# Optimization experiments

Measured on AMD Instinct MI355X. Metric: run time of the kernel, lower is better.

## Reference

```python
import jax, jax.numpy as jnp
import numpy as np

GRID = 20            # grid_size -> n1 = 400 nodes
CTX = 64             # context_size
HID = 10 * CTX       # hidden_dim per module code
BATCH = 256
K_ITERS = 100        # Dykstra iterations approximating the exact QP solve
LEAKY_SLOPE = 0.1


def _grid_incidence(g):
    """Incidence matrix of g x g grid DAG with right/down edges (SPO benchmark)."""
    n1 = g * g
    edges = []
    for i in range(g):
        for j in range(g):
            u = i * g + j
            if j + 1 < g:
                edges.append((u, u + 1))   # right
            if i + 1 < g:
                edges.append((u, u + g))   # down
    n2 = len(edges)
    A = np.zeros((n1, n2), dtype=np.float32)
    for e, (u, v) in enumerate(edges):
        A[u, e] = 1.0    # flow leaves u
        A[v, e] = -1.0   # flow enters v
    b = np.zeros(n1, dtype=np.float32)
    b[0] = 1.0           # source
    b[-1] = -1.0         # sink
    return A, b


def setup_inputs() -> dict:
    key = jax.random.key(0)
    ks = jax.random.split(key, 5)
    A_np, b_np = _grid_incidence(GRID)
    n2 = A_np.shape[1]
    d = jax.random.normal(ks[0], (BATCH, CTX), dtype=jnp.float32)
    W1 = jax.random.normal(ks[1], (CTX, HID), dtype=jnp.float32) / np.sqrt(CTX)
    b1 = jax.random.normal(ks[2], (HID,), dtype=jnp.float32) * 0.01
    W2 = jax.random.normal(ks[3], (HID, n2), dtype=jnp.float32) / np.sqrt(HID)
    b2 = jax.random.normal(ks[4], (n2,), dtype=jnp.float32) * 0.01
    return {
        "d": d, "W1": W1, "b1": b1, "W2": W2, "b2": b2,
        "A": jnp.asarray(A_np), "b_eq": jnp.asarray(b_np),
    }


def _solve_qp(w, A, b_eq):
    """Batched min_x w'x + 0.5||x||^2 s.t. Ax=b, x>=0 == proj of -w onto the
    feasible set, via Dykstra alternating projections (affine set / orthant)."""
    M = jnp.linalg.pinv(A @ A.T)  # [n1, n1]; AA' is the grid Laplacian (rank n1-1)

    def proj_affine(x):           # x: [B, n2]
        resid = x @ A.T - b_eq    # [B, n1]
        return x - (resid @ M) @ A

    y0 = -w                       # point to project
    p0 = jnp.zeros_like(w)
    q0 = jnp.zeros_like(w)

    def step(carry, _):
        y, p, q = carry
        t = y + p
        yp = proj_affine(t)
        p = t - yp
        t2 = yp + q
        y = jnp.maximum(t2, 0.0)  # projection onto x >= 0
        q = t2 - y
        return (y, p, q), None

    (y, _, _), _ = jax.lax.scan(step, (y0, p0, q0), None, length=K_ITERS)
    return y


def reference(d, W1, b1, W2, b2, A, b_eq):
    h = d @ W1 + b1
    h = jnp.where(h > 0, h, LEAKY_SLOPE * h)   # LeakyReLU(0.1)
    w = h @ W2 + b2                            # predicted edge costs [B, n2]
    return _solve_qp(w, A, b_eq)               # training-mode output: QP solution
```

## Files before the change

kernel.cpp:

```cpp
#include <hip/hip_runtime.h>
#include <math.h>

#define G 20
#define N1 400
#define N2 760
#define CTXS 64
#define HID 640
#define NB 256
#define ITERS 100
#define PI_D 3.14159265358979323846

__global__ __launch_bounds__(256, 1) void spnet_kernel(
    const float* __restrict__ dmat, const float* __restrict__ W1,
    const float* __restrict__ b1v, const float* __restrict__ W2,
    const float* __restrict__ b2v, const float* __restrict__ beq,
    float* __restrict__ out)
{
  const int tid = threadIdx.x;
  const int bb  = blockIdx.x;

  __shared__ __align__(16) float sV[N1];
  __shared__ __align__(16) float sdrow[CTXS];
  __shared__ __align__(16) float sh[HID];
  __shared__ __align__(16) float st0[N2];
  __shared__ __align__(16) float tRs[G][G];
  __shared__ __align__(16) float tDs[21][G];
  __shared__ __align__(16) float srow[G][G];
  __shared__ __align__(16) float T1T[G][G];
  __shared__ __align__(16) float T2T[G][G];
  __shared__ __align__(16) float W3m[G][G];
  __shared__ __align__(16) float Zs[G][G];

  for (int t = tid; t < N1; t += 256) {
    int k = t / G, i = t - G * k;
    double nk = (k == 0) ? 0.22360679774997896 : 0.31622776601683794;
    sV[t] = (float)(nk * cos(PI_D * (double)(k * (2 * i + 1)) / 40.0));
    ((float*)tRs)[t] = 0.f;
  }
  for (int t = tid; t < 21 * G; t += 256) ((float*)tDs)[t] = 0.f;
  if (tid < CTXS) sdrow[tid] = dmat[bb * CTXS + tid];
  __syncthreads();

  if (tid < HID / 4) {
    float4 acc = *(const float4*)(b1v + 4 * tid);
#pragma unroll 4
    for (int k = 0; k < CTXS; k += 4) {
      float4 h4 = *(const float4*)(sdrow + k);
      const float* wb = W1 + k * HID + 4 * tid;
      float4 w0 = *(const float4*)(wb);
      float4 w1 = *(const float4*)(wb + HID);
      float4 w2 = *(const float4*)(wb + 2 * HID);
      float4 w3 = *(const float4*)(wb + 3 * HID);
      acc.x = fmaf(h4.x, w0.x, acc.x); acc.y = fmaf(h4.x, w0.y, acc.y);
      acc.z = fmaf(h4.x, w0.z, acc.z); acc.w = fmaf(h4.x, w0.w, acc.w);
      acc.x = fmaf(h4.y, w1.x, acc.x); acc.y = fmaf(h4.y, w1.y, acc.y);
      acc.z = fmaf(h4.y, w1.z, acc.z); acc.w = fmaf(h4.y, w1.w, acc.w);
      acc.x = fmaf(h4.z, w2.x, acc.x); acc.y = fmaf(h4.z, w2.y, acc.y);
      acc.z = fmaf(h4.z, w2.z, acc.z); acc.w = fmaf(h4.z, w2.w, acc.w);
      acc.x = fmaf(h4.w, w3.x, acc.x); acc.y = fmaf(h4.w, w3.y, acc.y);
      acc.z = fmaf(h4.w, w3.z, acc.z); acc.w = fmaf(h4.w, w3.w, acc.w);
    }
    acc.x = acc.x > 0.f ? acc.x : 0.1f * acc.x;
    acc.y = acc.y > 0.f ? acc.y : 0.1f * acc.y;
    acc.z = acc.z > 0.f ? acc.z : 0.1f * acc.z;
    acc.w = acc.w > 0.f ? acc.w : 0.1f * acc.w;
    *(float4*)(sh + 4 * tid) = acc;
  }
  __syncthreads();

  if (tid < N2 / 4) {
    float4 acc = *(const float4*)(b2v + 4 * tid);
#pragma unroll 2
    for (int k = 0; k < HID; k += 4) {
      float4 h4 = *(const float4*)(sh + k);
      const float* wb = W2 + k * N2 + 4 * tid;
      float4 w0 = *(const float4*)(wb);
      float4 w1 = *(const float4*)(wb + N2);
      float4 w2 = *(const float4*)(wb + 2 * N2);
      float4 w3 = *(const float4*)(wb + 3 * N2);
      acc.x = fmaf(h4.x, w0.x, acc.x); acc.y = fmaf(h4.x, w0.y, acc.y);
      acc.z = fmaf(h4.x, w0.z, acc.z); acc.w = fmaf(h4.x, w0.w, acc.w);
      acc.x = fmaf(h4.y, w1.x, acc.x); acc.y = fmaf(h4.y, w1.y, acc.y);
      acc.z = fmaf(h4.y, w1.z, acc.z); acc.w = fmaf(h4.y, w1.w, acc.w);
      acc.x = fmaf(h4.z, w2.x, acc.x); acc.y = fmaf(h4.z, w2.y, acc.y);
      acc.z = fmaf(h4.z, w2.z, acc.z); acc.w = fmaf(h4.z, w2.w, acc.w);
      acc.x = fmaf(h4.w, w3.x, acc.x); acc.y = fmaf(h4.w, w3.y, acc.y);
      acc.z = fmaf(h4.w, w3.z, acc.z); acc.w = fmaf(h4.w, w3.w, acc.w);
    }
    float4 s; s.x = -acc.x; s.y = -acc.y; s.z = -acc.z; s.w = -acc.w;
    *(float4*)(st0 + 4 * tid) = s;
  }
  __syncthreads();

  const bool isD = (tid < 100);
  const int  rid = tid - 128;
  const bool isR = (rid >= 0 && rid < 100);

  const int dx  = tid % G;
  const int dk0 = 4 * (tid / G);
  float Vr[4][G], Vc[4][G], Sv[4];
  if (isD) {
#pragma unroll
    for (int a = 0; a < 4; ++a) {
      int k = dk0 + a;
#pragma unroll
      for (int m = 0; m < G; ++m) { Vr[a][m] = sV[k * G + m]; Vc[a][m] = sV[m * G + k]; }
      double lk = 2.0 - 2.0 * cos(PI_D * (double)k / 20.0);
      double lx = 2.0 - 2.0 * cos(PI_D * (double)dx / 20.0);
      Sv[a] = (k == 0 && dx == 0) ? 0.f : (float)(1.0 / (lk + lx));
    }
  }

  const int di = tid / 5, dj4 = (tid % 5) * 4;
  const bool dAct = isD && (di < 19);
  float dT[4], dQ[4], dY[4];
  if (dAct) {
#pragma unroll
    for (int m = 0; m < 4; ++m) {
      int j = dj4 + m;
      int e = (j < 19) ? (39 * di + 2 * j + 1) : (39 * di + 38);
      dT[m] = st0[e]; dQ[m] = 0.f; dY[m] = 0.f;
    }
    float4 w4 = {dT[0], dT[1], dT[2], dT[3]};
    *(float4*)&tDs[di + 1][dj4] = w4;
  }

  const int ri = rid / 5, rj4 = (rid % 5) * 4;
  float rT[4], rQ[4], rY[4]; float4 bq4 = {0.f, 0.f, 0.f, 0.f};
  if (isR) {
#pragma unroll
    for (int m = 0; m < 4; ++m) {
      int j = rj4 + m;
      if (j < 19) {
        int e = (ri < 19) ? (39 * ri + 2 * j) : (741 + j);
        rT[m] = st0[e];
      } else rT[m] = 0.f;
      rQ[m] = 0.f; rY[m] = 0.f;
    }
    float4 w4 = {rT[0], rT[1], rT[2], rT[3]};
    *(float4*)&tRs[ri][rj4] = w4;
    bq4 = *(const float4*)(beq + ri * G + rj4);
  }
  __syncthreads();

  for (int it = 0; it < ITERS; ++it) {
    if (isR) {
      float4 oR = *(const float4*)&tRs[ri][rj4];
      float  lf = (rj4 > 0) ? tRs[ri][rj4 - 1] : 0.f;
      float4 oD = *(const float4*)&tDs[ri + 1][rj4];
      float4 iD = *(const float4*)&tDs[ri][rj4];
      float4 r4;
      r4.x = oR.x + oD.x - lf   - iD.x - bq4.x;
      r4.y = oR.y + oD.y - oR.x - iD.y - bq4.y;
      r4.z = oR.z + oD.z - oR.y - iD.z - bq4.z;
      r4.w = oR.w + oD.w - oR.z - iD.w - bq4.w;
      *(float4*)&srow[ri][rj4] = r4;
    }
    __syncthreads();

    if (isD) {
      const float4* Rp = (const float4*)&srow[dx][0];
      float4 a0 = Rp[0], a1 = Rp[1], a2 = Rp[2], a3 = Rp[3], a4 = Rp[4];
      float rr[G] = {a0.x,a0.y,a0.z,a0.w, a1.x,a1.y,a1.z,a1.w, a2.x,a2.y,a2.z,a2.w,
                     a3.x,a3.y,a3.z,a3.w, a4.x,a4.y,a4.z,a4.w};
#pragma unroll
      for (int a = 0; a < 4; ++a) {
        float acc = 0.f;
#pragma unroll
        for (int m = 0; m < G; ++m) acc = fmaf(Vr[a][m], rr[m], acc);
        T1T[dk0 + a][dx] = acc;
      }
    }
    __syncthreads();

    if (isD) {
      const float4* Rp = (const float4*)&T1T[dx][0];
      float4 a0 = Rp[0], a1 = Rp[1], a2 = Rp[2], a3 = Rp[3], a4 = Rp[4];
      float rr[G] = {a0.x,a0.y,a0.z,a0.w, a1.x,a1.y,a1.z,a1.w, a2.x,a2.y,a2.z,a2.w,
                     a3.x,a3.y,a3.z,a3.w, a4.x,a4.y,a4.z,a4.w};
      float o[4];
#pragma unroll
      for (int a = 0; a < 4; ++a) {
        float acc = 0.f;
#pragma unroll
        for (int m = 0; m < G; ++m) acc = fmaf(Vr[a][m], rr[m], acc);
        o[a] = acc * Sv[a];
      }
      float4 w4 = {o[0], o[1], o[2], o[3]};
      *(float4*)&T2T[dx][dk0] = w4;
    }
    __syncthreads();

    if (isD) {
      const float4* Rp = (const float4*)&T2T[dx][0];
      float4 a0 = Rp[0], a1 = Rp[1], a2 = Rp[2], a3 = Rp[3], a4 = Rp[4];
      float rr[G] = {a0.x,a0.y,a0.z,a0.w, a1.x,a1.y,a1.z,a1.w, a2.x,a2.y,a2.z,a2.w,
                     a3.x,a3.y,a3.z,a3.w, a4.x,a4.y,a4.z,a4.w};
#pragma unroll
      for (int a = 0; a < 4; ++a) {
        float acc = 0.f;
#pragma unroll
        for (int m = 0; m < G; ++m) acc = fmaf(Vc[a][m], rr[m], acc);
        W3m[dk0 + a][dx] = acc;
      }
    }
    __syncthreads();

    if (isD) {
      const float4* Rp = (const float4*)&W3m[dx][0];
      float4 a0 = Rp[0], a1 = Rp[1], a2 = Rp[2], a3 = Rp[3], a4 = Rp[4];
      float rr[G] = {a0.x,a0.y,a0.z,a0.w, a1.x,a1.y,a1.z,a1.w, a2.x,a2.y,a2.z,a2.w,
                     a3.x,a3.y,a3.z,a3.w, a4.x,a4.y,a4.z,a4.w};
      float o[4];
#pragma unroll
      for (int a = 0; a < 4; ++a) {
        float acc = 0.f;
#pragma unroll
        for (int m = 0; m < G; ++m) acc = fmaf(Vc[a][m], rr[m], acc);
        o[a] = acc;
      }
      float4 w4 = {o[0], o[1], o[2], o[3]};
      *(float4*)&Zs[dx][dk0] = w4;
    }
    __syncthreads();

    if (isR) {
      float4 z4 = *(const float4*)&Zs[ri][rj4];
      float  zR = (rj4 < 16) ? Zs[ri][rj4 + 4] : 0.f;
      float pn[4] = {z4.x - z4.y, z4.y - z4.z, z4.z - z4.w, z4.w - zR};
      if (rj4 == 16) pn[3] = 0.f;
#pragma unroll
      for (int m = 0; m < 4; ++m) {
        float t2 = rT[m] - pn[m] + rQ[m];
        float yn = fmaxf(t2, 0.f);
        rQ[m] = t2 - yn; rY[m] = yn; rT[m] = yn + pn[m];
      }
      float4 w4 = {rT[0], rT[1], rT[2], rT[3]};
      *(float4*)&tRs[ri][rj4] = w4;
    }
    if (dAct) {
      float4 z4 = *(const float4*)&Zs[di][dj4];
      float4 zb = *(const float4*)&Zs[di + 1][dj4];
      float pn[4] = {z4.x - zb.x, z4.y - zb.y, z4.z - zb.z, z4.w - zb.w};
#pragma unroll
      for (int m = 0; m < 4; ++m) {
        float t2 = dT[m] - pn[m] + dQ[m];
        float yn = fmaxf(t2, 0.f);
        dQ[m] = t2 - yn; dY[m] = yn; dT[m] = yn + pn[m];
      }
      float4 w4 = {dT[0], dT[1], dT[2], dT[3]};
      *(float4*)&tDs[di + 1][dj4] = w4;
    }
    __syncthreads();
  }

  if (isR) {
#pragma unroll
    for (int m = 0; m < 4; ++m) {
      int j = rj4 + m;
      if (j < 19) {
        int e = (ri < 19) ? (39 * ri + 2 * j) : (741 + j);
        out[bb * N2 + e] = rY[m];
      }
    }
  }
  if (dAct) {
#pragma unroll
    for (int m = 0; m < 4; ++m) {
      int j = dj4 + m;
      int e = (j < 19) ? (39 * di + 2 * j + 1) : (39 * di + 38);
      out[bb * N2 + e] = dY[m];
    }
  }
}

extern "C" void kernel_launch(void* const* d_in, const int* in_sizes, int n_in,
                              void* d_out, int out_size, void* d_ws, size_t ws_size,
                              hipStream_t stream) {
  const float* d   = (const float*)d_in[0];
  const float* W1  = (const float*)d_in[1];
  const float* b1  = (const float*)d_in[2];
  const float* W2  = (const float*)d_in[3];
  const float* b2  = (const float*)d_in[4];
  const float* beq = (const float*)d_in[6];
  float* out = (float*)d_out;
  spnet_kernel<<<NB, 256, 0, stream>>>(d, W1, b1, W2, b2, beq, out);
}
```

Baseline: 221.0 us.

## Split MLP and Dykstra kernels, use even/odd DCT symmetry with 200 threads

```diff
diff --git a/kernel.cpp b/kernel.cpp
--- a/kernel.cpp
+++ b/kernel.cpp
@@ -8,39 +8,31 @@
 #define HID 640
 #define NB 256
 #define ITERS 100
-#define PI_D 3.14159265358979323846
-
-__global__ __launch_bounds__(256, 1) void spnet_kernel(
+#define PI_F 3.14159265358979323846f
+
+__device__ __forceinline__ int eR(int i, int j) { return (i < 19) ? (39 * i + 2 * j) : (741 + j); }
+__device__ __forceinline__ int eD(int i, int j) { return (j < 19) ? (39 * i + 2 * j + 1) : (39 * i + 38); }
+
+#define LOAD_ROW20(dst, base) do {                                          \
+    const float4* _rp = (const float4*)(base);                              \
+    float4 _r0 = _rp[0], _r1 = _rp[1], _r2 = _rp[2], _r3 = _rp[3], _r4 = _rp[4]; \
+    dst[0]=_r0.x; dst[1]=_r0.y; dst[2]=_r0.z; dst[3]=_r0.w;                 \
+    dst[4]=_r1.x; dst[5]=_r1.y; dst[6]=_r1.z; dst[7]=_r1.w;                 \
+    dst[8]=_r2.x; dst[9]=_r2.y; dst[10]=_r2.z; dst[11]=_r2.w;               \
+    dst[12]=_r3.x; dst[13]=_r3.y; dst[14]=_r3.z; dst[15]=_r3.w;             \
+    dst[16]=_r4.x; dst[17]=_r4.y; dst[18]=_r4.z; dst[19]=_r4.w; } while (0)
+
+__global__ __launch_bounds__(256, 1) void mlp_kernel(
     const float* __restrict__ dmat, const float* __restrict__ W1,
     const float* __restrict__ b1v, const float* __restrict__ W2,
-    const float* __restrict__ b2v, const float* __restrict__ beq,
-    float* __restrict__ out)
+    const float* __restrict__ b2v, float* __restrict__ io)
 {
   const int tid = threadIdx.x;
   const int bb  = blockIdx.x;
-
-  __shared__ __align__(16) float sV[N1];
   __shared__ __align__(16) float sdrow[CTXS];
   __shared__ __align__(16) float sh[HID];
-  __shared__ __align__(16) float st0[N2];
-  __shared__ __align__(16) float tRs[G][G];
-  __shared__ __align__(16) float tDs[21][G];
-  __shared__ __align__(16) float srow[G][G];
-  __shared__ __align__(16) float T1T[G][G];
-  __shared__ __align__(16) float T2T[G][G];
-  __shared__ __align__(16) float W3m[G][G];
-  __shared__ __align__(16) float Zs[G][G];
-
-  for (int t = tid; t < N1; t += 256) {
-    int k = t / G, i = t - G * k;
-    double nk = (k == 0) ? 0.22360679774997896 : 0.31622776601683794;
-    sV[t] = (float)(nk * cos(PI_D * (double)(k * (2 * i + 1)) / 40.0));
-    ((float*)tRs)[t] = 0.f;
-  }
-  for (int t = tid; t < 21 * G; t += 256) ((float*)tDs)[t] = 0.f;
   if (tid < CTXS) sdrow[tid] = dmat[bb * CTXS + tid];
   __syncthreads();
-
   if (tid < HID / 4) {
     float4 acc = *(const float4*)(b1v + 4 * tid);
 #pragma unroll 4
@@ -67,7 +59,6 @@
     *(float4*)(sh + 4 * tid) = acc;
   }
   __syncthreads();
-
   if (tid < N2 / 4) {
     float4 acc = *(const float4*)(b2v + 4 * tid);
 #pragma unroll 2
@@ -88,58 +79,74 @@
       acc.z = fmaf(h4.w, w3.z, acc.z); acc.w = fmaf(h4.w, w3.w, acc.w);
     }
     float4 s; s.x = -acc.x; s.y = -acc.y; s.z = -acc.z; s.w = -acc.w;
-    *(float4*)(st0 + 4 * tid) = s;
-  }
-  __syncthreads();
-
-  const bool isD = (tid < 100);
+    *(float4*)(io + bb * N2 + 4 * tid) = s;
+  }
+}
+
+__global__ __launch_bounds__(256, 1) void dykstra_kernel(float* __restrict__ io)
+{
+  const int tid = threadIdx.x;
+  const int bb  = blockIdx.x;
+  float* mine = io + bb * N2;
+
+  __shared__ __align__(16) float srowT[N1];
+  __shared__ __align__(16) float sc1[N1];
+  __shared__ __align__(16) float sc2T[N1];
+  __shared__ __align__(16) float sd1[N1];
+  __shared__ __align__(16) float szz[N1];
+  __shared__ __align__(16) float tRs[G][G];
+  __shared__ __align__(16) float tDs[21][G];
+
+  for (int t = tid; t < N1; t += 256) ((float*)tRs)[t] = 0.f;
+  for (int t = tid; t < 21 * G; t += 256) ((float*)tDs)[t] = 0.f;
+
+  const bool isC = (tid < 200);
+  const int c  = tid / 10;
+  const int u  = tid % 10;
+  const int k0 = 2 * u;
+
+  float VA0[10], VA1[10], VC[20], S0, S1;
+  {
+    const float n0 = 0.22360679774997896f, nk = 0.31622776601683794f;
+#pragma unroll
+    for (int i = 0; i < 10; ++i) {
+      VA0[i] = ((k0 == 0) ? n0 : nk) * cosf((float)(k0 * (2 * i + 1)) * (PI_F / 40.f));
+      VA1[i] = nk * cosf((float)((k0 + 1) * (2 * i + 1)) * (PI_F / 40.f));
+    }
+#pragma unroll
+    for (int k = 0; k < 20; ++k)
+      VC[k] = ((k == 0) ? n0 : nk) * cosf((float)(k * (2 * u + 1)) * (PI_F / 40.f));
+    float lc = 2.f - 2.f * cosf((float)c * (PI_F / 20.f));
+    float l0 = 2.f - 2.f * cosf((float)k0 * (PI_F / 20.f));
+    float l1 = 2.f - 2.f * cosf((float)(k0 + 1) * (PI_F / 20.f));
+    S0 = (c == 0 && k0 == 0) ? 0.f : 1.f / (lc + l0);
+    S1 = 1.f / (lc + l1);
+  }
+
+  const int  di = tid / 5, dj4 = (tid % 5) * 4;
+  const bool dAct = (tid < 100) && (di < 19);
+  float dT[4], dQ[4], dY[4];
   const int  rid = tid - 128;
   const bool isR = (rid >= 0 && rid < 100);
-
-  const int dx  = tid % G;
-  const int dk0 = 4 * (tid / G);
-  float Vr[4][G], Vc[4][G], Sv[4];
-  if (isD) {
-#pragma unroll
-    for (int a = 0; a < 4; ++a) {
-      int k = dk0 + a;
-#pragma unroll
-      for (int m = 0; m < G; ++m) { Vr[a][m] = sV[k * G + m]; Vc[a][m] = sV[m * G + k]; }
-      double lk = 2.0 - 2.0 * cos(PI_D * (double)k / 20.0);
-      double lx = 2.0 - 2.0 * cos(PI_D * (double)dx / 20.0);
-      Sv[a] = (k == 0 && dx == 0) ? 0.f : (float)(1.0 / (lk + lx));
-    }
-  }
-
-  const int di = tid / 5, dj4 = (tid % 5) * 4;
-  const bool dAct = isD && (di < 19);
-  float dT[4], dQ[4], dY[4];
+  const int  ri = isR ? (rid / 5) : 0, rj4 = isR ? ((rid % 5) * 4) : 0;
+  float rT[4], rQ[4], rY[4];
+#pragma unroll
+  for (int m = 0; m < 4; ++m) { dT[m]=0.f; dQ[m]=0.f; dY[m]=0.f; rT[m]=0.f; rQ[m]=0.f; rY[m]=0.f; }
+
+  __syncthreads();
+
   if (dAct) {
 #pragma unroll
-    for (int m = 0; m < 4; ++m) {
-      int j = dj4 + m;
-      int e = (j < 19) ? (39 * di + 2 * j + 1) : (39 * di + 38);
-      dT[m] = st0[e]; dQ[m] = 0.f; dY[m] = 0.f;
-    }
-    float4 w4 = {dT[0], dT[1], dT[2], dT[3]};
-    *(float4*)&tDs[di + 1][dj4] = w4;
-  }
-
-  const int ri = rid / 5, rj4 = (rid % 5) * 4;
-  float rT[4], rQ[4], rY[4]; float4 bq4 = {0.f, 0.f, 0.f, 0.f};
+    for (int m = 0; m < 4; ++m) dT[m] = mine[eD(di, dj4 + m)];
+    *(float4*)&tDs[di + 1][dj4] = make_float4(dT[0], dT[1], dT[2], dT[3]);
+  }
   if (isR) {
 #pragma unroll
     for (int m = 0; m < 4; ++m) {
       int j = rj4 + m;
-      if (j < 19) {
-        int e = (ri < 19) ? (39 * ri + 2 * j) : (741 + j);
-        rT[m] = st0[e];
-      } else rT[m] = 0.f;
-      rQ[m] = 0.f; rY[m] = 0.f;
-    }
-    float4 w4 = {rT[0], rT[1], rT[2], rT[3]};
-    *(float4*)&tRs[ri][rj4] = w4;
-    bq4 = *(const float4*)(beq + ri * G + rj4);
+      rT[m] = (j < 19) ? mine[eR(ri, j)] : 0.f;
+    }
+    *(float4*)&tRs[ri][rj4] = make_float4(rT[0], rT[1], rT[2], rT[3]);
   }
   __syncthreads();
 
@@ -149,84 +156,76 @@
       float  lf = (rj4 > 0) ? tRs[ri][rj4 - 1] : 0.f;
       float4 oD = *(const float4*)&tDs[ri + 1][rj4];
       float4 iD = *(const float4*)&tDs[ri][rj4];
-      float4 r4;
-      r4.x = oR.x + oD.x - lf   - iD.x - bq4.x;
-      r4.y = oR.y + oD.y - oR.x - iD.y - bq4.y;
-      r4.z = oR.z + oD.z - oR.y - iD.z - bq4.z;
-      r4.w = oR.w + oD.w - oR.z - iD.w - bq4.w;
-      *(float4*)&srow[ri][rj4] = r4;
-    }
-    __syncthreads();
-
-    if (isD) {
-      const float4* Rp = (const float4*)&srow[dx][0];
-      float4 a0 = Rp[0], a1 = Rp[1], a2 = Rp[2], a3 = Rp[3], a4 = Rp[4];
-      float rr[G] = {a0.x,a0.y,a0.z,a0.w, a1.x,a1.y,a1.z,a1.w, a2.x,a2.y,a2.z,a2.w,
-                     a3.x,a3.y,a3.z,a3.w, a4.x,a4.y,a4.z,a4.w};
-#pragma unroll
-      for (int a = 0; a < 4; ++a) {
-        float acc = 0.f;
-#pragma unroll
-        for (int m = 0; m < G; ++m) acc = fmaf(Vr[a][m], rr[m], acc);
-        T1T[dk0 + a][dx] = acc;
-      }
-    }
-    __syncthreads();
-
-    if (isD) {
-      const float4* Rp = (const float4*)&T1T[dx][0];
-      float4 a0 = Rp[0], a1 = Rp[1], a2 = Rp[2], a3 = Rp[3], a4 = Rp[4];
-      float rr[G] = {a0.x,a0.y,a0.z,a0.w, a1.x,a1.y,a1.z,a1.w, a2.x,a2.y,a2.z,a2.w,
-                     a3.x,a3.y,a3.z,a3.w, a4.x,a4.y,a4.z,a4.w};
-      float o[4];
-#pragma unroll
-      for (int a = 0; a < 4; ++a) {
-        float acc = 0.f;
-#pragma unroll
-        for (int m = 0; m < G; ++m) acc = fmaf(Vr[a][m], rr[m], acc);
-        o[a] = acc * Sv[a];
-      }
-      float4 w4 = {o[0], o[1], o[2], o[3]};
-      *(float4*)&T2T[dx][dk0] = w4;
-    }
-    __syncthreads();
-
-    if (isD) {
-      const float4* Rp = (const float4*)&T2T[dx][0];
-      float4 a0 = Rp[0], a1 = Rp[1], a2 = Rp[2], a3 = Rp[3], a4 = Rp[4];
-      float rr[G] = {a0.x,a0.y,a0.z,a0.w, a1.x,a1.y,a1.z,a1.w, a2.x,a2.y,a2.z,a2.w,
-                     a3.x,a3.y,a3.z,a3.w, a4.x,a4.y,a4.z,a4.w};
-#pragma unroll
-      for (int a = 0; a < 4; ++a) {
-        float acc = 0.f;
-#pragma unroll
-        for (int m = 0; m < G; ++m) acc = fmaf(Vc[a][m], rr[m], acc);
-        W3m[dk0 + a][dx] = acc;
-      }
-    }
-    __syncthreads();
-
-    if (isD) {
-      const float4* Rp = (const float4*)&W3m[dx][0];
-      float4 a0 = Rp[0], a1 = Rp[1], a2 = Rp[2], a3 = Rp[3], a4 = Rp[4];
-      float rr[G] = {a0.x,a0.y,a0.z,a0.w, a1.x,a1.y,a1.z,a1.w, a2.x,a2.y,a2.z,a2.w,
-                     a3.x,a3.y,a3.z,a3.w, a4.x,a4.y,a4.z,a4.w};
-      float o[4];
-#pragma unroll
-      for (int a = 0; a < 4; ++a) {
-        float acc = 0.f;
-#pragma unroll
-        for (int m = 0; m < G; ++m) acc = fmaf(Vc[a][m], rr[m], acc);
-        o[a] = acc;
-      }
-      float4 w4 = {o[0], o[1], o[2], o[3]};
-      *(float4*)&Zs[dx][dk0] = w4;
+      float r0 = oR.x + oD.x - lf   - iD.x;
+      float r1 = oR.y + oD.y - oR.x - iD.y;
+      float r2 = oR.z + oD.z - oR.y - iD.z;
+      float r3 = oR.w + oD.w - oR.z - iD.w;
+      if (ri == 0  && rj4 == 0)  r0 -= 1.f;
+      if (ri == 19 && rj4 == 16) r3 += 1.f;
+      srowT[(rj4 + 0) * G + ri] = r0;
+      srowT[(rj4 + 1) * G + ri] = r1;
+      srowT[(rj4 + 2) * G + ri] = r2;
+      srowT[(rj4 + 3) * G + ri] = r3;
+    }
+    __syncthreads();
+
+    if (isC) {
+      float d_[20]; LOAD_ROW20(d_, srowT + 20 * c);
+      float a0 = 0.f, a1 = 0.f;
+#pragma unroll
+      for (int i = 0; i < 10; ++i) {
+        float e_ = d_[i] + d_[19 - i], o_ = d_[i] - d_[19 - i];
+        a0 = fmaf(VA0[i], e_, a0);
+        a1 = fmaf(VA1[i], o_, a1);
+      }
+      sc1[k0 * G + c] = a0;
+      sc1[(k0 + 1) * G + c] = a1;
+    }
+    __syncthreads();
+
+    if (isC) {
+      float d_[20]; LOAD_ROW20(d_, sc1 + 20 * c);
+      float a0 = 0.f, a1 = 0.f;
+#pragma unroll
+      for (int j = 0; j < 10; ++j) {
+        float e_ = d_[j] + d_[19 - j], o_ = d_[j] - d_[19 - j];
+        a0 = fmaf(VA0[j], e_, a0);
+        a1 = fmaf(VA1[j], o_, a1);
+      }
+      sc2T[k0 * G + c] = a0 * S0;
+      sc2T[(k0 + 1) * G + c] = a1 * S1;
+    }
+    __syncthreads();
+
+    if (isC) {
+      float d_[20]; LOAD_ROW20(d_, sc2T + 20 * c);
+      float E = 0.f, O = 0.f;
+#pragma unroll
+      for (int m = 0; m < 10; ++m) {
+        E = fmaf(VC[2 * m], d_[2 * m], E);
+        O = fmaf(VC[2 * m + 1], d_[2 * m + 1], O);
+      }
+      sd1[u * G + c] = E + O;
+      sd1[(19 - u) * G + c] = E - O;
+    }
+    __syncthreads();
+
+    if (isC) {
+      float d_[20]; LOAD_ROW20(d_, sd1 + 20 * c);
+      float E = 0.f, O = 0.f;
+#pragma unroll
+      for (int m = 0; m < 10; ++m) {
+        E = fmaf(VC[2 * m], d_[2 * m], E);
+        O = fmaf(VC[2 * m + 1], d_[2 * m + 1], O);
+      }
+      szz[c * G + u] = E + O;
+      szz[c * G + (19 - u)] = E - O;
     }
     __syncthreads();
 
     if (isR) {
-      float4 z4 = *(const float4*)&Zs[ri][rj4];
-      float  zR = (rj4 < 16) ? Zs[ri][rj4 + 4] : 0.f;
+      float4 z4 = *(const float4*)&szz[ri * G + rj4];
+      float  zR = (rj4 < 16) ? szz[ri * G + rj4 + 4] : 0.f;
       float pn[4] = {z4.x - z4.y, z4.y - z4.z, z4.z - z4.w, z4.w - zR};
       if (rj4 == 16) pn[3] = 0.f;
 #pragma unroll
@@ -235,12 +234,11 @@
         float yn = fmaxf(t2, 0.f);
         rQ[m] = t2 - yn; rY[m] = yn; rT[m] = yn + pn[m];
       }
-      float4 w4 = {rT[0], rT[1], rT[2], rT[3]};
-      *(float4*)&tRs[ri][rj4] = w4;
+      *(float4*)&tRs[ri][rj4] = make_float4(rT[0], rT[1], rT[2], rT[3]);
     }
     if (dAct) {
-      float4 z4 = *(const float4*)&Zs[di][dj4];
-      float4 zb = *(const float4*)&Zs[di + 1][dj4];
+      float4 z4 = *(const float4*)&szz[di * G + dj4];
+      float4 zb = *(const float4*)&szz[(di + 1) * G + dj4];
       float pn[4] = {z4.x - zb.x, z4.y - zb.y, z4.z - zb.z, z4.w - zb.w};
 #pragma unroll
       for (int m = 0; m < 4; ++m) {
@@ -248,8 +246,7 @@
         float yn = fmaxf(t2, 0.f);
         dQ[m] = t2 - yn; dY[m] = yn; dT[m] = yn + pn[m];
       }
-      float4 w4 = {dT[0], dT[1], dT[2], dT[3]};
-      *(float4*)&tDs[di + 1][dj4] = w4;
+      *(float4*)&tDs[di + 1][dj4] = make_float4(dT[0], dT[1], dT[2], dT[3]);
     }
     __syncthreads();
   }
@@ -258,19 +255,12 @@
 #pragma unroll
     for (int m = 0; m < 4; ++m) {
       int j = rj4 + m;
-      if (j < 19) {
-        int e = (ri < 19) ? (39 * ri + 2 * j) : (741 + j);
-        out[bb * N2 + e] = rY[m];
-      }
+      if (j < 19) mine[eR(ri, j)] = rY[m];
     }
   }
   if (dAct) {
 #pragma unroll
-    for (int m = 0; m < 4; ++m) {
-      int j = dj4 + m;
-      int e = (j < 19) ? (39 * di + 2 * j + 1) : (39 * di + 38);
-      out[bb * N2 + e] = dY[m];
-    }
+    for (int m = 0; m < 4; ++m) mine[eD(di, dj4 + m)] = dY[m];
   }
 }
 
@@ -282,7 +272,7 @@
   const float* b1  = (const float*)d_in[2];
   const float* W2  = (const float*)d_in[3];
   const float* b2  = (const float*)d_in[4];
-  const float* beq = (const float*)d_in[6];
-  float* out = (float*)d_out;
-  spnet_kernel<<<NB, 256, 0, stream>>>(d, W1, b1, W2, b2, beq, out);
+  float* io = (float*)d_out;
+  mlp_kernel<<<NB, 256, 0, stream>>>(d, W1, b1, W2, b2, io);
+  dykstra_kernel<<<NB, 256, 0, stream>>>(io);
 }
```

Result: faster. 214.9 us (-2.8%).
